# Optimization experiments

Measured on AMD Instinct MI355X. Metric: run time of the kernel, lower is better.

Reference implementation:

```python
import jax, jax.numpy as jnp
import numpy as np

# SRU config from the module: 3 layers, highway_bias=0, rescale=True, no layer_norm.
# rescale factor from sru package: sqrt(1 + exp(highway_bias)*2)
SCALE_X = (1.0 + np.exp(0.0) * 2.0) ** 0.5

IMG_DIM, T, HID, NCLS, B = 512, 12, 1024, 51, 2048


def _sru_layer(x, W, vc, b):
    # x: (T, B, d_in); W: (d_in, k*d); vc: (2, d) gate-recurrence vectors; b: (2, d) biases
    Tn, Bn, d_in = x.shape
    d = vc.shape[1]
    k = W.shape[1] // d  # 4 if d_in != d else 3
    U = jnp.einsum('tbi,ij->tbj', x, W).reshape(Tn, Bn, k, d)
    u0, u1, u2 = U[:, :, 0], U[:, :, 1], U[:, :, 2]
    resid = U[:, :, 3] if k == 4 else x  # projected residual when dims differ
    vf, vr = vc[0], vc[1]
    bf, br = b[0], b[1]

    def step(c, inp):
        u0t, u1t, u2t, xt = inp
        f = jax.nn.sigmoid(u1t + vf * c + bf)          # forget gate (uses c_{t-1})
        c_new = f * c + (1.0 - f) * u0t                # cell update
        r = jax.nn.sigmoid(u2t + vr * c_new + br)      # reset gate (uses c_t, as in SRU CUDA)
        h = r * jnp.tanh(c_new) + (1.0 - r) * xt * SCALE_X  # highway with rescale
        return c_new, h

    c0 = jnp.zeros((Bn, d), x.dtype)
    c_last, h = jax.lax.scan(step, c0, (u0, u1, u2, resid))
    return h, c_last


def setup_inputs() -> dict:
    key = jax.random.key(0)
    ks = jax.random.split(key, 12)
    inp = {}
    inp['x'] = jax.random.normal(ks[0], (B, T, IMG_DIM), jnp.float32)
    # layer 0: 512 -> 1024, k=4; layers 1,2: 1024 -> 1024, k=3
    inp['W0'] = jax.random.normal(ks[1], (IMG_DIM, 4 * HID), jnp.float32) / np.sqrt(IMG_DIM)
    inp['W1'] = jax.random.normal(ks[2], (HID, 3 * HID), jnp.float32) / np.sqrt(HID)
    inp['W2'] = jax.random.normal(ks[3], (HID, 3 * HID), jnp.float32) / np.sqrt(HID)
    inp['vc0'] = jax.random.normal(ks[4], (2, HID), jnp.float32) * 0.1
    inp['vc1'] = jax.random.normal(ks[5], (2, HID), jnp.float32) * 0.1
    inp['vc2'] = jax.random.normal(ks[6], (2, HID), jnp.float32) * 0.1
    inp['b0'] = jnp.zeros((2, HID), jnp.float32)
    inp['b1'] = jnp.zeros((2, HID), jnp.float32)
    inp['b2'] = jnp.zeros((2, HID), jnp.float32)
    inp['fc_w'] = jax.random.normal(ks[7], (HID, NCLS), jnp.float32) / np.sqrt(HID)
    inp['fc_b'] = jnp.zeros((NCLS,), jnp.float32)
    return inp


def reference(x, W0, W1, W2, vc0, vc1, vc2, b0, b1, b2, fc_w, fc_b):
    h = jnp.transpose(x, (1, 0, 2))  # (T, B, img_dim)
    for W, vc, b in ((W0, vc0, b0), (W1, vc1, b1), (W2, vc2, b2)):
        h, _ = _sru_layer(h, W, vc, b)
    # dropout layers are identity in eval mode
    logits = jnp.einsum('tbh,hc->tbc', h, fc_w) + fc_b  # (T, B, num_class)
    return jnp.mean(logits, axis=0)  # (B, num_class)
```

## Files before the change

### kernel.cpp

```cpp
#include <hip/hip_runtime.h>
#include <math.h>

#define TSTEPS 12
#define BATCH  2048
#define IMG    512
#define HIDN   1024
#define NCLASS 51
#define SCALE_X 1.7320508075688772f

typedef __attribute__((ext_vector_type(8)))  _Float16 f16x8;
typedef __attribute__((ext_vector_type(2)))  _Float16 f16x2;
typedef __attribute__((ext_vector_type(16))) float    f32x16;

__device__ __forceinline__ float sigf(float x) {
    return 1.f / (1.f + __expf(-x));
}

#define VMCNT_IMM(n) (0x0F70 | (n))


template<int TJ, int NCOMP>
__global__ __launch_bounds__(256, 2)
void gemm_sru(const _Float16* __restrict__ A, const _Float16* __restrict__ Bt,
              const _Float16* __restrict__ resid,
              const float* __restrict__ vc, const float* __restrict__ bias,
              _Float16* __restrict__ hout, float* __restrict__ hbar, int K,
              int pcshift) {
    constexpr int BN    = 64 * TJ;
    constexpr int NCH   = BN / NCOMP;
    constexpr int ATILE = 192 * 32;
    constexpr int BTILE = BN * 32;
    constexpr int S_A3  = 3 * ATILE;
    constexpr int EPAD  = BN + 8;
    constexpr int EPI   = 96 * EPAD;
    constexpr int HREG  = 96 * NCH;
    constexpr int KTH   = NCH / 16;
    constexpr int PAIRS = NCH / 2;
    constexpr int STG   = 3 * (ATILE + BTILE);
    constexpr int TOT   = STG > (EPI + HREG) ? STG : (EPI + HREG);
    __shared__ __align__(16) _Float16 smem[TOT];

    const int tid  = threadIdx.x;
    const int lane = tid & 63;
    const int w    = tid >> 6;

    const int nbx = gridDim.x;
    const int b   = blockIdx.y * nbx + blockIdx.x;
    const int pc1 = (nbx >> 3) - 1;
    const int xk  = b & 7, s = b >> 3;
    const int bx  = xk + ((s & pc1) << 3);
    const int by  = s >> pcshift;

    const int bm  = by * 192;
    const int KT  = K >> 4;

    const bool isA = (w < 2);
    const int  nst = isA ? 3 : TJ;
    const _Float16* gsrc = isA ? A : Bt;
    const int rt0g = (isA ? (bm >> 5) : (bx * (BN >> 5))) + (w & 1) * nst;
    const _Float16* gbase = gsrc + (size_t)rt0g * KT * 512 + (lane << 3);
    const int lds0  = isA ? 0 : S_A3;
    const int ltile = isA ? ATILE : BTILE;
    const int lhalf = (w & 1) * nst * 1024;

    auto stage = [&](int buf, int k0) {
        const _Float16* g = gbase + (size_t)(k0 >> 4) * 512;
        _Float16* l = smem + lds0 + buf * ltile + lhalf;
        for (int i = 0; i < nst; ++i)
            #pragma unroll
            for (int kt = 0; kt < 2; ++kt)
                __builtin_amdgcn_global_load_lds(
                    (const __attribute__((address_space(1))) unsigned int*)(g + ((size_t)i * KT + kt) * 512),
                    (__attribute__((address_space(3))) unsigned int*)(l + (i * 2 + kt) * 512),
                    16, 0, 0);
    };

    const int wy32 = (w >> 1) * 3;
    const int wx32 = (w & 1) * TJ;
    const int l5   = lane >> 5;
    const int m32  = lane & 31;

    f32x16 acc[3][TJ];
    #pragma unroll
    for (int i = 0; i < 3; ++i)
        #pragma unroll
        for (int j = 0; j < TJ; ++j)
            #pragma unroll
            for (int r = 0; r < 16; ++r) acc[i][j][r] = 0.f;

    stage(0, 0);
    stage(1, 32);
    int bi = 0;
    for (int k0 = 0; k0 < K; k0 += 32) {
        if (k0 + 32 < K) {
            if (isA) __builtin_amdgcn_s_waitcnt(VMCNT_IMM(6));
            else     __builtin_amdgcn_s_waitcnt(VMCNT_IMM(2 * TJ));
        } else {
            __builtin_amdgcn_s_waitcnt(VMCNT_IMM(0));
        }
        __builtin_amdgcn_s_barrier();
        if (k0 + 64 < K) {
            int nb = bi + 2; if (nb >= 3) nb -= 3;
            stage(nb, k0 + 64);
        }

        const _Float16* la = smem + bi * ATILE;
        const _Float16* lb = smem + S_A3 + bi * BTILE;
        #pragma unroll
        for (int ks = 0; ks < 2; ++ks) {
            f16x8 a[3], bfr[TJ];
            #pragma unroll
            for (int i = 0; i < 3; ++i)
                a[i] = *(const f16x8*)&la[((wy32 + i) * 2 + ks) * 512 + (lane << 3)];
            #pragma unroll
            for (int j = 0; j < TJ; ++j)
                bfr[j] = *(const f16x8*)&lb[((wx32 + j) * 2 + ks) * 512 + (lane << 3)];
            #pragma unroll
            for (int i = 0; i < 3; ++i)
                #pragma unroll
                for (int j = 0; j < TJ; ++j)
                    acc[i][j] = __builtin_amdgcn_mfma_f32_32x32x16_f16(
                        a[i], bfr[j], acc[i][j], 0, 0, 0);
        }
        ++bi; if (bi == 3) bi = 0;
    }

    _Float16 (*uld)[EPAD] = (_Float16 (*)[EPAD])smem;
    _Float16* hreg = smem + EPI;
    const int bl   = tid / PAIRS;
    const int pr   = tid % PAIRS;
    const int gcol = bx * NCH + pr * 2;

    #pragma unroll
    for (int pass = 0; pass < 2; ++pass) {
        __syncthreads();
        if ((w >> 1) == pass) {
            #pragma unroll
            for (int i = 0; i < 3; ++i)
                #pragma unroll
                for (int j = 0; j < TJ; ++j)
                    #pragma unroll
                    for (int r = 0; r < 16; ++r) {
                        const int row = i * 32 + (r & 3) + 8 * (r >> 2) + 4 * l5;
                        uld[row][(wx32 + j) * 32 + m32] = (_Float16)acc[i][j][r];
                    }
        }
        __syncthreads();

        if (tid < 8 * PAIRS) {
            const float2 vf  = *(const float2*)&vc[gcol];
            const float2 vr  = *(const float2*)&vc[HIDN + gcol];
            const float2 bfv = *(const float2*)&bias[gcol];
            const float2 brv = *(const float2*)&bias[HIDN + gcol];
            const int ca = (pr * 2) * NCOMP, cb = (pr * 2 + 1) * NCOMP;

            float c0 = 0.f, c1 = 0.f, s0 = 0.f, s1 = 0.f;
            #pragma unroll
            for (int t = 0; t < TSTEPS; ++t) {
                const int row = bl * 12 + t;
                const float u0a = (float)uld[row][ca + 0];
                const float u1a = (float)uld[row][ca + 1];
                const float u2a = (float)uld[row][ca + 2];
                const float u0b = (float)uld[row][cb + 0];
                const float u1b = (float)uld[row][cb + 1];
                const float u2b = (float)uld[row][cb + 2];
                float xta, xtb;
                if (NCOMP == 4) {
                    xta = (float)uld[row][ca + 3];
                    xtb = (float)uld[row][cb + 3];
                } else {
                    const int grow = bm + pass * 96 + row;
                    const size_t gran = ((size_t)(grow >> 5) * KT + (gcol >> 4)) * 512
                                      + (size_t)((grow & 31) + ((gcol >> 3) & 1) * 32) * 8
                                      + (gcol & 7);
                    const f16x2 xv = *(const f16x2*)&resid[gran];
                    xta = (float)xv[0]; xtb = (float)xv[1];
                }

                const float f0 = sigf(u1a + vf.x * c0 + bfv.x);
                c0 = f0 * c0 + (1.f - f0) * u0a;
                const float r0_ = sigf(u2a + vr.x * c0 + brv.x);
                const float th0 = 2.f * sigf(2.f * c0) - 1.f;
                const float hv0 = r0_ * th0 + (1.f - r0_) * xta * SCALE_X;

                const float f1 = sigf(u1b + vf.y * c1 + bfv.y);
                c1 = f1 * c1 + (1.f - f1) * u0b;
                const float r1_ = sigf(u2b + vr.y * c1 + brv.y);
                const float th1 = 2.f * sigf(2.f * c1) - 1.f;
                const float hv1 = r1_ * th1 + (1.f - r1_) * xtb * SCALE_X;

                if (hout) {
                    const int rtl  = row >> 5;
                    const int ktl  = pr >> 3;
                    const int lloc = (row & 31) + ((pr >> 2) & 1) * 32;
                    f16x2 hv = { (_Float16)hv0, (_Float16)hv1 };
                    *(f16x2*)&hreg[(rtl * KTH + ktl) * 512 + lloc * 8 + (pr & 3) * 2] = hv;
                }
                s0 += hv0; s1 += hv1;
            }
            if (hbar) {
                const int gb = bm / 12 + pass * 8 + bl;
                *(float2*)&hbar[(size_t)gb * HIDN + gcol] =
                    make_float2(s0 * (1.f / TSTEPS), s1 * (1.f / TSTEPS));
            }
        }

        if (hout) {
            __syncthreads();
            const int rtg0 = (bm + pass * 96) >> 5;
            for (int g = tid; g < HREG / 8; g += 256) {
                const int c = g >> 6, l = g & 63;
                const f16x8 v = *(const f16x8*)&hreg[c * 512 + l * 8];
                const int rtl = c / KTH, ktl = c % KTH;
                const size_t gc = (size_t)(rtg0 + rtl) * 64 + bx * KTH + ktl;
                *(f16x8*)&hout[gc * 512 + l * 8] = v;
            }
        }
    }
}

template<int NC>
__global__ __launch_bounds__(256)
void wsplit_t(const float* __restrict__ W, _Float16* __restrict__ Wt, int K) {
    __shared__ _Float16 tile[32][132];
    const int N  = NC * 1024;
    const int KT = K >> 4;
    const int rt = blockIdx.x, kc = blockIdx.y;

    const int nl = threadIdx.x & 31;
    const int kl = threadIdx.x >> 5;
    const int np = rt * 32 + nl;
    const int h  = np / NC, comp = np - h * NC;
    const int n  = comp * 1024 + h;
    #pragma unroll
    for (int kk = 0; kk < 16; ++kk) {
        const int k = kc * 128 + kl * 16 + kk;
        tile[nl][kl * 16 + kk] = (_Float16)W[(size_t)k * N + n];
    }
    __syncthreads();

    #pragma unroll
    for (int p = 0; p < 2; ++p) {
        const int slot = p * 256 + threadIdx.x;
        const int ktl  = slot >> 6, l = slot & 63;
        f16x8 v;
        #pragma unroll
        for (int j = 0; j < 8; ++j)
            v[j] = tile[l & 31][ktl * 16 + ((l >> 5) << 3) + j];
        const int kt = kc * 8 + ktl;
        *(f16x8*)&Wt[((size_t)rt * KT + kt) * 512 + l * 8] = v;
    }
}

__global__ __launch_bounds__(256)
void esplit(const float* __restrict__ src, _Float16* __restrict__ dst) {
    __shared__ _Float16 tile[32][132];
    const int rt = blockIdx.x, kc = blockIdx.y;
    const int kli = threadIdx.x & 31;
    const int rl  = threadIdx.x >> 5;
    #pragma unroll
    for (int rr = 0; rr < 4; ++rr) {
        const int row = rl * 4 + rr;
        const float4 v = *(const float4*)&src[(size_t)(rt * 32 + row) * 512 + kc * 128 + kli * 4];
        tile[row][kli * 4 + 0] = (_Float16)v.x;
        tile[row][kli * 4 + 1] = (_Float16)v.y;
        tile[row][kli * 4 + 2] = (_Float16)v.z;
        tile[row][kli * 4 + 3] = (_Float16)v.w;
    }
    __syncthreads();

    #pragma unroll
    for (int p = 0; p < 2; ++p) {
        const int slot = p * 256 + threadIdx.x;
        const int ktl  = slot >> 6, l = slot & 63;
        f16x8 v;
        #pragma unroll
        for (int j = 0; j < 8; ++j)
            v[j] = tile[l & 31][ktl * 16 + ((l >> 5) << 3) + j];
        const int kt = kc * 8 + ktl;
        *(f16x8*)&dst[((size_t)rt * 32 + kt) * 512 + l * 8] = v;
    }
}

__global__ __launch_bounds__(64)
void final_fc(const float* __restrict__ hbar, const float* __restrict__ fcw,
              const float* __restrict__ fcb, float* __restrict__ out) {
    __shared__ float hrow[HIDN];
    const int b = blockIdx.x;
    for (int i = threadIdx.x; i < HIDN; i += 64)
        hrow[i] = hbar[(size_t)b * HIDN + i];
    __syncthreads();

    const int c = threadIdx.x;
    if (c < NCLASS) {
        float acc = fcb[c];
        #pragma unroll 8
        for (int k = 0; k < HIDN; ++k)
            acc = fmaf(hrow[k], fcw[(size_t)k * NCLASS + c], acc);
        out[(size_t)b * NCLASS + c] = acc;
    }
}

extern "C" void kernel_launch(void* const* d_in, const int* in_sizes, int n_in,
                              void* d_out, int out_size, void* d_ws, size_t ws_size,
                              hipStream_t stream) {
    const float* x   = (const float*)d_in[0];
    const float* W0  = (const float*)d_in[1];
    const float* W1  = (const float*)d_in[2];
    const float* W2  = (const float*)d_in[3];
    const float* vc0 = (const float*)d_in[4];
    const float* vc1 = (const float*)d_in[5];
    const float* vc2 = (const float*)d_in[6];
    const float* b0  = (const float*)d_in[7];
    const float* b1  = (const float*)d_in[8];
    const float* b2  = (const float*)d_in[9];
    const float* fcw = (const float*)d_in[10];
    const float* fcb = (const float*)d_in[11];
    float* out = (float*)d_out;

    char* ws = (char*)d_ws;
    size_t off = 0;
    auto carve = [&](size_t bytes) { char* p = ws + off; off = (off + bytes + 255) & ~255ull; return p; };

    _Float16* W0t = (_Float16*)carve((size_t)4096 * 512 * 2);
    _Float16* W1t = (_Float16*)carve((size_t)3072 * 1024 * 2);
    _Float16* W2t = (_Float16*)carve((size_t)3072 * 1024 * 2);
    const size_t W_BYTES = off;

    const size_t PER_B = 12ull * 512 * 2 + 2ull * 12 * 1024 * 2 + 1024ull * 4 + 1024;
    int CB = 32;
    if      (W_BYTES + 2048ull * PER_B <= ws_size) CB = 2048;
    else if (W_BYTES + 1024ull * PER_B <= ws_size) CB = 1024;
    else if (W_BYTES +  512ull * PER_B <= ws_size) CB = 512;
    else if (W_BYTES +  256ull * PER_B <= ws_size) CB = 256;
    else if (W_BYTES +  128ull * PER_B <= ws_size) CB = 128;
    else if (W_BYTES +   64ull * PER_B <= ws_size) CB = 64;
    const int MC = CB * TSTEPS;

    _Float16* x16  = (_Float16*)carve((size_t)MC * 512 * 2);
    _Float16* hA16 = (_Float16*)carve((size_t)MC * 1024 * 2);
    _Float16* hB16 = (_Float16*)carve((size_t)MC * 1024 * 2);
    float*    hbar = (float*)carve((size_t)CB * 1024 * 4);

    const dim3 blk256(256);

    wsplit_t<4><<<dim3(4096 / 32, 512 / 128),  blk256, 0, stream>>>(W0, W0t, 512);
    wsplit_t<3><<<dim3(3072 / 32, 1024 / 128), blk256, 0, stream>>>(W1, W1t, 1024);
    wsplit_t<3><<<dim3(3072 / 32, 1024 / 128), blk256, 0, stream>>>(W2, W2t, 1024);

    for (int cb = 0; cb < BATCH / CB; ++cb) {
        const float* xc   = x   + (size_t)cb * CB * TSTEPS * IMG;
        float*       outc = out + (size_t)cb * CB * NCLASS;

        esplit<<<dim3(MC / 32, 4), blk256, 0, stream>>>(xc, x16);
        gemm_sru<2, 4><<<dim3(4096 / 128, MC / 192), blk256, 0, stream>>>(
            x16, W0t, nullptr, vc0, b0, hA16, nullptr, 512, 2);

        gemm_sru<3, 3><<<dim3(3072 / 192, MC / 192), blk256, 0, stream>>>(
            hA16, W1t, hA16, vc1, b1, hB16, nullptr, 1024, 1);

        gemm_sru<3, 3><<<dim3(3072 / 192, MC / 192), blk256, 0, stream>>>(
            hB16, W2t, hB16, vc2, b2, nullptr, hbar, 1024, 1);

        final_fc<<<dim3(CB), dim3(64), 0, stream>>>(hbar, fcw, fcb, outc);
    }
}
```

Baseline: 776.3 us.

## Load B fragments directly into registers, stage only A through LDS

The GEMM mainloop stops staging the B (weight) tile through shared memory. Each wave now loads its B fragments straight from global memory into double-buffered registers one K-step ahead. All four waves share the A staging into LDS, which now uses four buffers instead of three, and the K loop is unrolled by four so buffer indices are compile-time constants. This cuts LDS traffic and footprint, but B is now fetched separately by each wave that uses it, global load volume rises, and the register buffers for B add pressure on VGPRs.

New measurement: 748.1 us. 1.04x faster.

```diff
diff --git a/kernel.cpp b/kernel.cpp
--- a/kernel.cpp
+++ b/kernel.cpp
@@ -29,14 +29,12 @@
     constexpr int BN    = 64 * TJ;
     constexpr int NCH   = BN / NCOMP;
     constexpr int ATILE = 192 * 32;
-    constexpr int BTILE = BN * 32;
-    constexpr int S_A3  = 3 * ATILE;
     constexpr int EPAD  = BN + 8;
     constexpr int EPI   = 96 * EPAD;
     constexpr int HREG  = 96 * NCH;
     constexpr int KTH   = NCH / 16;
     constexpr int PAIRS = NCH / 2;
-    constexpr int STG   = 3 * (ATILE + BTILE);
+    constexpr int STG   = 4 * ATILE;
     constexpr int TOT   = STG > (EPI + HREG) ? STG : (EPI + HREG);
     __shared__ __align__(16) _Float16 smem[TOT];
 
@@ -54,25 +52,18 @@
     const int bm  = by * 192;
     const int KT  = K >> 4;
 
-    const bool isA = (w < 2);
-    const int  nst = isA ? 3 : TJ;
-    const _Float16* gsrc = isA ? A : Bt;
-    const int rt0g = (isA ? (bm >> 5) : (bx * (BN >> 5))) + (w & 1) * nst;
-    const _Float16* gbase = gsrc + (size_t)rt0g * KT * 512 + (lane << 3);
-    const int lds0  = isA ? 0 : S_A3;
-    const int ltile = isA ? ATILE : BTILE;
-    const int lhalf = (w & 1) * nst * 1024;
-
-    auto stage = [&](int buf, int k0) {
-        const _Float16* g = gbase + (size_t)(k0 >> 4) * 512;
-        _Float16* l = smem + lds0 + buf * ltile + lhalf;
-        for (int i = 0; i < nst; ++i)
-            #pragma unroll
-            for (int kt = 0; kt < 2; ++kt)
-                __builtin_amdgcn_global_load_lds(
-                    (const __attribute__((address_space(1))) unsigned int*)(g + ((size_t)i * KT + kt) * 512),
-                    (__attribute__((address_space(3))) unsigned int*)(l + (i * 2 + kt) * 512),
-                    16, 0, 0);
+    const int rt0 = bm >> 5;
+    auto stageA = [&](int buf, int k0) {
+        const int kt0 = k0 >> 4;
+        #pragma unroll
+        for (int i = 0; i < 3; ++i) {
+            const int L = w * 3 + i, rc = L >> 1, kk = L & 1;
+            const _Float16* g = A + ((size_t)(rt0 + rc) * KT + kt0 + kk) * 512 + (lane << 3);
+            __builtin_amdgcn_global_load_lds(
+                (const __attribute__((address_space(1))) unsigned int*)g,
+                (__attribute__((address_space(3))) unsigned int*)(smem + buf * ATILE + L * 512),
+                16, 0, 0);
+        }
     };
 
     const int wy32 = (w >> 1) * 3;
@@ -80,6 +71,18 @@
     const int l5   = lane >> 5;
     const int m32  = lane & 31;
 
+    const _Float16* bglob = Bt + (size_t)(bx * (BN >> 5) + wx32) * KT * 512 + (lane << 3);
+
+    f16x8 bfr[2][2][TJ];
+    auto loadB = [&](int k0, int slot) {
+        const int kt0 = k0 >> 4;
+        #pragma unroll
+        for (int ks = 0; ks < 2; ++ks)
+            #pragma unroll
+            for (int j = 0; j < TJ; ++j)
+                bfr[slot][ks][j] = *(const f16x8*)&bglob[((size_t)j * KT + kt0 + ks) * 512];
+    };
+
     f32x16 acc[3][TJ];
     #pragma unroll
     for (int i = 0; i < 3; ++i)
@@ -88,41 +91,35 @@
             #pragma unroll
             for (int r = 0; r < 16; ++r) acc[i][j][r] = 0.f;
 
-    stage(0, 0);
-    stage(1, 32);
-    int bi = 0;
-    for (int k0 = 0; k0 < K; k0 += 32) {
-        if (k0 + 32 < K) {
-            if (isA) __builtin_amdgcn_s_waitcnt(VMCNT_IMM(6));
-            else     __builtin_amdgcn_s_waitcnt(VMCNT_IMM(2 * TJ));
-        } else {
-            __builtin_amdgcn_s_waitcnt(VMCNT_IMM(0));
-        }
-        __builtin_amdgcn_s_barrier();
-        if (k0 + 64 < K) {
-            int nb = bi + 2; if (nb >= 3) nb -= 3;
-            stage(nb, k0 + 64);
-        }
-
-        const _Float16* la = smem + bi * ATILE;
-        const _Float16* lb = smem + S_A3 + bi * BTILE;
-        #pragma unroll
-        for (int ks = 0; ks < 2; ++ks) {
-            f16x8 a[3], bfr[TJ];
-            #pragma unroll
-            for (int i = 0; i < 3; ++i)
-                a[i] = *(const f16x8*)&la[((wy32 + i) * 2 + ks) * 512 + (lane << 3)];
-            #pragma unroll
-            for (int j = 0; j < TJ; ++j)
-                bfr[j] = *(const f16x8*)&lb[((wx32 + j) * 2 + ks) * 512 + (lane << 3)];
-            #pragma unroll
-            for (int i = 0; i < 3; ++i)
+    stageA(0, 0);
+    stageA(1, 32);
+    loadB(0, 0);
+
+    for (int K0 = 0; K0 < K; K0 += 128) {
+        #pragma unroll
+        for (int u = 0; u < 4; ++u) {
+            const int k0 = K0 + u * 32;
+            if (k0 + 32 < K) __builtin_amdgcn_s_waitcnt(VMCNT_IMM(3 + 2 * TJ));
+            else             __builtin_amdgcn_s_waitcnt(VMCNT_IMM(2 * TJ));
+            __builtin_amdgcn_s_barrier();
+            if (k0 + 64 < K) stageA((u + 2) & 3, k0 + 64);
+            if (k0 + 32 < K) loadB(k0 + 32, (u + 1) & 1);
+
+            const _Float16* la = smem + u * ATILE;
+            #pragma unroll
+            for (int ks = 0; ks < 2; ++ks) {
+                f16x8 a[3];
                 #pragma unroll
-                for (int j = 0; j < TJ; ++j)
-                    acc[i][j] = __builtin_amdgcn_mfma_f32_32x32x16_f16(
-                        a[i], bfr[j], acc[i][j], 0, 0, 0);
-        }
-        ++bi; if (bi == 3) bi = 0;
+                for (int i = 0; i < 3; ++i)
+                    a[i] = *(const f16x8*)&la[((wy32 + i) * 2 + ks) * 512 + (lane << 3)];
+                #pragma unroll
+                for (int i = 0; i < 3; ++i)
+                    #pragma unroll
+                    for (int j = 0; j < TJ; ++j)
+                        acc[i][j] = __builtin_amdgcn_mfma_f32_32x32x16_f16(
+                            a[i], bfr[u & 1][ks][j], acc[i][j], 0, 0, 0);
+            }
+        }
     }
 
     _Float16 (*uld)[EPAD] = (_Float16 (*)[EPAD])smem;
```
